# Kernel optimization log

Hardware: AMD Instinct MI355X
Metric: run time of the kernel (lower is better)

Reference implementation:

```python
import jax, jax.numpy as jnp
import numpy as np

HEADS = 4

def _axial_attn(xs, wqkv, wproj, bproj, heads=HEADS):
    # xs: [B', C, L]; wqkv: [3C, C]; wproj: [C, C]; bproj: [C]
    Bp, C, L = xs.shape
    hd = C // heads
    scale = hd ** -0.5
    qkv = jnp.einsum('oc,bcl->bol', wqkv, xs)  # [B', 3C, L]
    q, k, v = jnp.split(qkv, 3, axis=1)
    q = q.reshape(Bp, heads, hd, L)
    k = k.reshape(Bp, heads, hd, L)
    v = v.reshape(Bp, heads, hd, L)
    attn = jax.nn.softmax(jnp.einsum('bhdi,bhdj->bhij', q, k) * scale, axis=-1)
    out = jnp.einsum('bhij,bhdj->bhdi', attn, v).reshape(Bp, C, L)
    return jnp.einsum('oc,bcl->bol', wproj, out) + bproj[None, :, None]

def setup_inputs() -> dict:
    key = jax.random.key(0)
    ks = jax.random.split(key, 7)
    B, C, H, W = 8, 128, 128, 128
    return {
        'x': jax.random.normal(ks[0], (B, C, H, W), dtype=jnp.float32),
        'wqkv_h': jax.random.normal(ks[1], (3 * C, C), dtype=jnp.float32) * 0.05,
        'wproj_h': jax.random.normal(ks[2], (C, C), dtype=jnp.float32) * 0.05,
        'bproj_h': jax.random.normal(ks[3], (C,), dtype=jnp.float32) * 0.05,
        'wqkv_w': jax.random.normal(ks[4], (3 * C, C), dtype=jnp.float32) * 0.05,
        'wproj_w': jax.random.normal(ks[5], (C, C), dtype=jnp.float32) * 0.05,
        'bproj_w': jax.random.normal(ks[6], (C,), dtype=jnp.float32) * 0.05,
    }

def reference(x, wqkv_h, wproj_h, bproj_h, wqkv_w, wproj_w, bproj_w):
    B, C, H, W = x.shape
    # height pass: rows become batch, attend along W
    xh = x.transpose(0, 2, 1, 3).reshape(B * H, C, W)
    xh = _axial_attn(xh, wqkv_h, wproj_h, bproj_h)
    xh = xh.reshape(B, H, C, W).transpose(0, 2, 1, 3)
    # width pass: cols become batch, attend along H
    xw = x.transpose(0, 3, 1, 2).reshape(B * W, C, H)
    xw = _axial_attn(xw, wqkv_w, wproj_w, bproj_w)
    xw = xw.reshape(B, W, C, H).transpose(0, 2, 3, 1)
    return (xh + xw) / 2
```

## Files before the change

kernel.cpp:

```cpp
#include <hip/hip_runtime.h>
#include <hip/hip_bf16.h>
#include <stdint.h>

typedef __attribute__((ext_vector_type(8))) short short8v;
typedef __attribute__((ext_vector_type(4))) float f32x4;
typedef unsigned short u16;
typedef unsigned int u32;

__device__ __align__(16) u16 g_xTw[8u * 128u * 128u * 128u];
__device__ __align__(16) u16 g_W2[8u * 128u * 128u * 128u];
__device__ __align__(16) u16 g_wqkvP[2u * 49152u];
__device__ __align__(16) u16 g_wpP[2u * 16384u];

#define XST_OFF 0
#define QT_OFF  32768
#define KT_OFF  43008
#define VH_OFF  53248
#define OT_OFF  61952
#define SMEM_BYTES 72192

__device__ __forceinline__ u16 f2bf(float f) {
    u32 b = __float_as_uint(f);
    b += 0x7FFFu + ((b >> 16) & 1u);
    return (u16)(b >> 16);
}
__device__ __forceinline__ u32 pk2(float a, float b) {
    __hip_bfloat162 h = __float22bfloat162_rn(make_float2(a, b));
    union { __hip_bfloat162 h; u32 u; } cv; cv.h = h; return cv.u;
}
__device__ __forceinline__ float bf2f(u16 u) {
    return __uint_as_float(((u32)u) << 16);
}

__global__ __launch_bounds__(512)
void prep_weights(const float* __restrict__ wqkv_h, const float* __restrict__ wproj_h,
                  const float* __restrict__ wqkv_w, const float* __restrict__ wproj_w)
{
    const float QSC = 0.17677669529663687f;
    int id = blockIdx.x * 512 + threadIdx.x;
    if (id < 12288) {
        int p = id / 6144, i2 = id % 6144;
        int h = i2 / 1536, i3 = i2 % 1536;
        int t = i3 / 256,  i4 = i3 % 256;
        int kk = i4 / 64,  lane = i4 % 64;
        int cc = lane & 15, qq = lane >> 4;
        int r96 = t * 16 + cc;
        int g = r96 >> 5, rl = r96 & 31;
        const float* src = (p == 0 ? wqkv_h : wqkv_w) + (g * 128 + h * 32 + rl) * 128 + kk * 32 + qq * 8;
        float4 a = *(const float4*)src;
        float4 c = *(const float4*)(src + 4);
        float s = (g == 0) ? QSC : 1.0f;
        *(uint4*)(g_wqkvP + (size_t)id * 8) =
            make_uint4(pk2(a.x * s, a.y * s), pk2(a.z * s, a.w * s),
                       pk2(c.x * s, c.y * s), pk2(c.z * s, c.w * s));
    } else {
        int id2 = id - 12288;
        int p = id2 / 2048, i2 = id2 % 2048;
        int h = i2 / 512,  i3 = i2 % 512;
        int t = i3 / 64,   lane = i3 % 64;
        int cc = lane & 15, qq = lane >> 4;
        int o = t * 16 + cc;
        const float* src = (p == 0 ? wproj_h : wproj_w) + o * 128 + h * 32 + qq * 8;
        float4 a = *(const float4*)src;
        float4 c = *(const float4*)(src + 4);
        *(uint4*)(g_wpP + (size_t)id2 * 8) =
            make_uint4(pk2(a.x, a.y), pk2(a.z, a.w), pk2(c.x, c.y), pk2(c.z, c.w));
    }
}

__global__ __launch_bounds__(256)
void transpose_x(const float* __restrict__ x)
{
    __shared__ char tsm[32768];
    const int b = blockIdx.x >> 6;
    const int hp = blockIdx.x & 63;
    const int tid = threadIdx.x;
    for (int hh = 0; hh < 2; ++hh) {
        const int h = hp * 2 + hh;
        #pragma unroll
        for (int it = 0; it < 16; ++it) {
            int task = it * 256 + tid;
            int w = task & 127, c4 = task >> 7;
            const float* p = x + (size_t)b * 2097152 + (c4 * 4) * 16384 + h * 128 + w;
            u32 u0 = pk2(p[0], p[16384]);
            u32 u1 = pk2(p[2 * 16384], p[3 * 16384]);
            int off = w * 256 + ((((c4 >> 1) << 4) ^ ((w & 7) << 4)) | ((c4 & 1) << 3));
            *(uint2*)(tsm + off) = make_uint2(u0, u1);
        }
        __syncthreads();
        #pragma unroll
        for (int it = 0; it < 8; ++it) {
            int i = it * 256 + tid;
            int w = i >> 4, c8 = i & 15;
            uint4 v = *(const uint4*)(tsm + w * 256 + ((c8 << 4) ^ ((w & 7) << 4)));
            size_t ds = ((size_t)(b * 128 + w) * 128 + h) * 128 + (((c8 << 4) ^ ((h & 7) << 4)) >> 1);
            *(uint4*)(g_xTw + ds) = v;
        }
        __syncthreads();
    }
}

template<int GATHER, int DMODE>
__global__ __launch_bounds__(512, 4)
void attn_kernel(const float* __restrict__ srcx, int pass,
                 const float* __restrict__ bias, float* __restrict__ out)
{
    extern __shared__ char smem[];
    const int t    = threadIdx.x;
    const int lane = t & 63;
    const int wv   = t >> 6;
    const int cc   = lane & 15;
    const int qq   = lane >> 4;
    const int b    = blockIdx.x >> 7;
    const int row  = blockIdx.x & 127;
    const f32x4 zf4 = (f32x4){0.f, 0.f, 0.f, 0.f};

    if constexpr (GATHER) {
        #pragma unroll
        for (int it = 0; it < 4; ++it) {
            int task = t + 512 * it;
            int l = task & 127, c8 = task >> 7;
            const float* p = srcx + (size_t)b * 2097152 + (c8 * 8) * 16384 + row * 128 + l;
            u32 u0 = pk2(p[0], p[16384]);
            u32 u1 = pk2(p[2 * 16384], p[3 * 16384]);
            u32 u2 = pk2(p[4 * 16384], p[5 * 16384]);
            u32 u3 = pk2(p[6 * 16384], p[7 * 16384]);
            *(uint4*)(smem + XST_OFF + l * 256 + ((c8 * 16) ^ ((l & 7) << 4))) = make_uint4(u0, u1, u2, u3);
        }
    } else {
        const u16* slab = g_xTw + (size_t)(b * 128 + row) * 16384;
        #pragma unroll
        for (int it = 0; it < 4; ++it) {
            int idx = t + 512 * it;
            *(uint4*)(smem + XST_OFF + idx * 16) = *(const uint4*)(slab + idx * 8);
        }
    }

    float biasr[4];
    #pragma unroll
    for (int r = 0; r < 4; ++r) biasr[r] = bias[wv * 16 + 4 * qq + r];

    f32x4 yacc[8];
    #pragma unroll
    for (int i = 0; i < 8; ++i) yacc[i] = zf4;

    __syncthreads();

    const int og = wv & 1;
    const int lg = wv >> 1;

    for (int h = 0; h < 4; ++h) {
        const u16* wb  = g_wqkvP + (size_t)(pass * 4 + h) * 12288;
        const u16* wpb = g_wpP   + (size_t)(pass * 4 + h) * 4096 + (wv * 64 + lane) * 8;

        {
            f32x4 acc[3][2];
            #pragma unroll
            for (int ot = 0; ot < 3; ++ot)
                #pragma unroll
                for (int lt = 0; lt < 2; ++lt) acc[ot][lt] = zf4;
            #pragma unroll
            for (int kk = 0; kk < 4; ++kk) {
                short8v A[3], Bf[2];
                #pragma unroll
                for (int ot = 0; ot < 3; ++ot)
                    A[ot] = *(const short8v*)(wb + (((og * 3 + ot) * 4 + kk) * 64 + lane) * 8);
                #pragma unroll
                for (int lt = 0; lt < 2; ++lt) {
                    int l = lg * 32 + lt * 16 + cc;
                    Bf[lt] = *(const short8v*)(smem + XST_OFF + l * 256 + (((kk * 64 + qq * 16)) ^ ((l & 7) << 4)));
                }
                #pragma unroll
                for (int ot = 0; ot < 3; ++ot)
                    #pragma unroll
                    for (int lt = 0; lt < 2; ++lt)
                        acc[ot][lt] = __builtin_amdgcn_mfma_f32_16x16x32_bf16(A[ot], Bf[lt], acc[ot][lt], 0, 0, 0);
            }
            #pragma unroll
            for (int ot = 0; ot < 3; ++ot) {
                int got = og * 3 + ot;
                #pragma unroll
                for (int lt = 0; lt < 2; ++lt) {
                    int l0 = (lg * 2 + lt) * 16 + cc;
                    f32x4 v = acc[ot][lt];
                    if (got < 2) {
                        *(uint2*)(smem + QT_OFF + l0 * 80 + (got * 16 + 4 * qq) * 2) =
                            make_uint2(pk2(v[0], v[1]), pk2(v[2], v[3]));
                    } else if (got < 4) {
                        *(uint2*)(smem + KT_OFF + l0 * 80 + ((got - 2) * 16 + 4 * qq) * 2) =
                            make_uint2(pk2(v[0], v[1]), pk2(v[2], v[3]));
                    } else {
                        int d0 = (got - 4) * 16 + 4 * qq;
                        #pragma unroll
                        for (int r = 0; r < 4; ++r)
                            *(u16*)(smem + VH_OFF + (d0 + r) * 272 + l0 * 2) = f2bf(v[r]);
                    }
                }
            }
        }
        __syncthreads();

        f32x4 sacc[8];
        {
            short8v aq = *(const short8v*)(smem + QT_OFF + (wv * 16 + cc) * 80 + qq * 16);
            #pragma unroll
            for (int jt = 0; jt < 8; ++jt) {
                short8v bk = *(const short8v*)(smem + KT_OFF + (jt * 16 + cc) * 80 + qq * 16);
                sacc[jt] = __builtin_amdgcn_mfma_f32_16x16x32_bf16(bk, aq, zf4, 0, 0, 0);
            }
        }
        float mx = -3.4e38f;
        #pragma unroll
        for (int jt = 0; jt < 8; ++jt)
            #pragma unroll
            for (int r = 0; r < 4; ++r) mx = fmaxf(mx, sacc[jt][r]);
        mx = fmaxf(mx, __shfl_xor(mx, 16));
        mx = fmaxf(mx, __shfl_xor(mx, 32));
        float sm = 0.f;
        #pragma unroll
        for (int jt = 0; jt < 8; ++jt)
            #pragma unroll
            for (int r = 0; r < 4; ++r) {
                float p = exp2f((sacc[jt][r] - mx) * 1.4426950408889634f);
                sacc[jt][r] = p;
                sm += p;
            }
        sm += __shfl_xor(sm, 16);
        sm += __shfl_xor(sm, 32);
        float rden = 1.0f / sm;
        u32 u[8][2];
        #pragma unroll
        for (int jt = 0; jt < 8; ++jt) {
            u[jt][0] = pk2(sacc[jt][0], sacc[jt][1]);
            u[jt][1] = pk2(sacc[jt][2], sacc[jt][3]);
        }

        f32x4 oacc[2] = {zf4, zf4};
        const int base = cc + ((qq & 1) << 5);
        const bool hiT = (qq >> 1) != 0;
        #pragma unroll
        for (int kt = 0; kt < 4; ++kt) {
            int a0 = __shfl((int)u[2 * kt][0], base),      a1 = __shfl((int)u[2 * kt][1], base);
            int a2 = __shfl((int)u[2 * kt][0], base + 16), a3 = __shfl((int)u[2 * kt][1], base + 16);
            int b0 = __shfl((int)u[2 * kt + 1][0], base),      b1 = __shfl((int)u[2 * kt + 1][1], base);
            int b2 = __shfl((int)u[2 * kt + 1][0], base + 16), b3 = __shfl((int)u[2 * kt + 1][1], base + 16);
            union { uint4 u4; short8v s8; } pf;
            pf.u4 = make_uint4((u32)(hiT ? b0 : a0), (u32)(hiT ? b1 : a1),
                               (u32)(hiT ? b2 : a2), (u32)(hiT ? b3 : a3));
            #pragma unroll
            for (int dt = 0; dt < 2; ++dt) {
                short8v vf = *(const short8v*)(smem + VH_OFF + (dt * 16 + cc) * 272 + kt * 64 + qq * 16);
                oacc[dt] = __builtin_amdgcn_mfma_f32_16x16x32_bf16(vf, pf.s8, oacc[dt], 0, 0, 0);
            }
        }
        #pragma unroll
        for (int dt = 0; dt < 2; ++dt) {
            *(uint2*)(smem + OT_OFF + (wv * 16 + cc) * 80 + (dt * 16 + 4 * qq) * 2) =
                make_uint2(pk2(oacc[dt][0] * rden, oacc[dt][1] * rden),
                           pk2(oacc[dt][2] * rden, oacc[dt][3] * rden));
        }
        __syncthreads();

        {
            short8v aw = *(const short8v*)wpb;
            #pragma unroll
            for (int it = 0; it < 8; ++it) {
                short8v of = *(const short8v*)(smem + OT_OFF + (it * 16 + cc) * 80 + qq * 16);
                yacc[it] = __builtin_amdgcn_mfma_f32_16x16x32_bf16(aw, of, yacc[it], 0, 0, 0);
            }
        }
    }

    #pragma unroll
    for (int it = 0; it < 8; ++it) {
        #pragma unroll
        for (int r = 0; r < 4; ++r) {
            float y = (yacc[it][r] + biasr[r]) * 0.5f;
            int o = wv * 16 + 4 * qq + r;
            int l = it * 16 + cc;
            size_t idx = ((size_t)(b * 128 + o) * 128 + row) * 128 + l;
            if constexpr (DMODE == 0) out[idx] = y;
            else                      g_W2[idx] = f2bf(y);
        }
    }
}

__global__ __launch_bounds__(256)
void merge_w(float* __restrict__ out)
{
    __shared__ char msm[128 * 264];
    const int b = blockIdx.x >> 7;
    const int o = blockIdx.x & 127;
    const int tid = threadIdx.x;
    const u16* slab = g_W2 + (size_t)(b * 128 + o) * 16384;
    #pragma unroll
    for (int it = 0; it < 8; ++it) {
        int i = it * 256 + tid;
        int w = i >> 4, h8 = i & 15;
        *(uint4*)(msm + w * 264 + h8 * 16) = *(const uint4*)(slab + w * 128 + h8 * 8);
    }
    __syncthreads();
    float* op = out + (size_t)(b * 128 + o) * 16384;
    #pragma unroll
    for (int it = 0; it < 8; ++it) {
        int i = it * 256 + tid;
        int h = i >> 4, w8 = i & 15;
        float f[8];
        #pragma unroll
        for (int k = 0; k < 8; ++k)
            f[k] = bf2f(*(const u16*)(msm + (w8 * 8 + k) * 264 + h * 2));
        float* dp = op + h * 128 + w8 * 8;
        float4 v0 = *(float4*)dp;
        float4 v1 = *(float4*)(dp + 4);
        v0.x += f[0]; v0.y += f[1]; v0.z += f[2]; v0.w += f[3];
        v1.x += f[4]; v1.y += f[5]; v1.z += f[6]; v1.w += f[7];
        *(float4*)dp = v0;
        *(float4*)(dp + 4) = v1;
    }
}

extern "C" void kernel_launch(void* const* d_in, const int* in_sizes, int n_in,
                              void* d_out, int out_size, void* d_ws, size_t ws_size,
                              hipStream_t stream)
{
    const float* x       = (const float*)d_in[0];
    const float* wqkv_h  = (const float*)d_in[1];
    const float* wproj_h = (const float*)d_in[2];
    const float* bproj_h = (const float*)d_in[3];
    const float* wqkv_w  = (const float*)d_in[4];
    const float* wproj_w = (const float*)d_in[5];
    const float* bproj_w = (const float*)d_in[6];
    float* out = (float*)d_out;

    (void)hipFuncSetAttribute((const void*)attn_kernel<1, 0>,
                              hipFuncAttributeMaxDynamicSharedMemorySize, SMEM_BYTES);
    (void)hipFuncSetAttribute((const void*)attn_kernel<0, 1>,
                              hipFuncAttributeMaxDynamicSharedMemorySize, SMEM_BYTES);

    prep_weights<<<dim3(32), dim3(512), 0, stream>>>(wqkv_h, wproj_h, wqkv_w, wproj_w);
    transpose_x<<<dim3(512), dim3(256), 0, stream>>>(x);
    attn_kernel<1, 0><<<dim3(1024), dim3(512), SMEM_BYTES, stream>>>(x, 0, bproj_h, out);
    attn_kernel<0, 1><<<dim3(1024), dim3(512), SMEM_BYTES, stream>>>(nullptr, 1, bproj_w, out);
    merge_w<<<dim3(1024), dim3(256), 0, stream>>>(out);
}
```

Baseline: 182.2 us.

## Merge both axial passes into one launch and stage bf16 height input

The transpose kernel now also writes a bf16 copy of x laid out per (batch,row) for the height pass. Both attention passes then run in a single 2048-block launch that picks pass, bias and destination from the block index, replacing the strided fp32 gather in pass 0 with a contiguous bf16 load. MFMA sections are wrapped in s_setprio raises so waves doing matrix math get issue priority. The cost is an extra 32 MB bf16 write in the transpose kernel, plus runtime branching where template specialisation used to decide pass behaviour.

```diff
diff --git a/kernel.cpp b/kernel.cpp
--- a/kernel.cpp
+++ b/kernel.cpp
@@ -7,10 +7,11 @@
 typedef unsigned short u16;
 typedef unsigned int u32;
 
+__device__ __align__(16) u16 g_xh [8u * 128u * 128u * 128u];
 __device__ __align__(16) u16 g_xTw[8u * 128u * 128u * 128u];
-__device__ __align__(16) u16 g_W2[8u * 128u * 128u * 128u];
+__device__ __align__(16) u16 g_W2 [8u * 128u * 128u * 128u];
 __device__ __align__(16) u16 g_wqkvP[2u * 49152u];
-__device__ __align__(16) u16 g_wpP[2u * 16384u];
+__device__ __align__(16) u16 g_wpP [2u * 16384u];
 
 #define XST_OFF 0
 #define QT_OFF  32768
@@ -91,6 +92,11 @@
         #pragma unroll
         for (int it = 0; it < 8; ++it) {
             int i = it * 256 + tid;
+            *(uint4*)(g_xh + (size_t)(b * 128 + h) * 16384 + i * 8) = *(const uint4*)(tsm + i * 16);
+        }
+        #pragma unroll
+        for (int it = 0; it < 8; ++it) {
+            int i = it * 256 + tid;
             int w = i >> 4, c8 = i & 15;
             uint4 v = *(const uint4*)(tsm + w * 256 + ((c8 << 4) ^ ((w & 7) << 4)));
             size_t ds = ((size_t)(b * 128 + w) * 128 + h) * 128 + (((c8 << 4) ^ ((h & 7) << 4)) >> 1);
@@ -100,10 +106,9 @@
     }
 }
 
-template<int GATHER, int DMODE>
 __global__ __launch_bounds__(512, 4)
-void attn_kernel(const float* __restrict__ srcx, int pass,
-                 const float* __restrict__ bias, float* __restrict__ out)
+void attn_kernel(const float* __restrict__ bias_h, const float* __restrict__ bias_w,
+                 float* __restrict__ out)
 {
     extern __shared__ char smem[];
     const int t    = threadIdx.x;
@@ -111,24 +116,13 @@
     const int wv   = t >> 6;
     const int cc   = lane & 15;
     const int qq   = lane >> 4;
-    const int b    = blockIdx.x >> 7;
+    const int pass = blockIdx.x >> 10;
+    const int b    = (blockIdx.x >> 7) & 7;
     const int row  = blockIdx.x & 127;
     const f32x4 zf4 = (f32x4){0.f, 0.f, 0.f, 0.f};
 
-    if constexpr (GATHER) {
-        #pragma unroll
-        for (int it = 0; it < 4; ++it) {
-            int task = t + 512 * it;
-            int l = task & 127, c8 = task >> 7;
-            const float* p = srcx + (size_t)b * 2097152 + (c8 * 8) * 16384 + row * 128 + l;
-            u32 u0 = pk2(p[0], p[16384]);
-            u32 u1 = pk2(p[2 * 16384], p[3 * 16384]);
-            u32 u2 = pk2(p[4 * 16384], p[5 * 16384]);
-            u32 u3 = pk2(p[6 * 16384], p[7 * 16384]);
-            *(uint4*)(smem + XST_OFF + l * 256 + ((c8 * 16) ^ ((l & 7) << 4))) = make_uint4(u0, u1, u2, u3);
-        }
-    } else {
-        const u16* slab = g_xTw + (size_t)(b * 128 + row) * 16384;
+    {
+        const u16* slab = (pass ? g_xTw : g_xh) + (size_t)(b * 128 + row) * 16384;
         #pragma unroll
         for (int it = 0; it < 4; ++it) {
             int idx = t + 512 * it;
@@ -136,6 +130,7 @@
         }
     }
 
+    const float* bias = pass ? bias_w : bias_h;
     float biasr[4];
     #pragma unroll
     for (int r = 0; r < 4; ++r) biasr[r] = bias[wv * 16 + 4 * qq + r];
@@ -159,6 +154,7 @@
             for (int ot = 0; ot < 3; ++ot)
                 #pragma unroll
                 for (int lt = 0; lt < 2; ++lt) acc[ot][lt] = zf4;
+            __builtin_amdgcn_s_setprio(1);
             #pragma unroll
             for (int kk = 0; kk < 4; ++kk) {
                 short8v A[3], Bf[2];
@@ -176,6 +172,7 @@
                     for (int lt = 0; lt < 2; ++lt)
                         acc[ot][lt] = __builtin_amdgcn_mfma_f32_16x16x32_bf16(A[ot], Bf[lt], acc[ot][lt], 0, 0, 0);
             }
+            __builtin_amdgcn_s_setprio(0);
             #pragma unroll
             for (int ot = 0; ot < 3; ++ot) {
                 int got = og * 3 + ot;
@@ -203,11 +200,13 @@
         f32x4 sacc[8];
         {
             short8v aq = *(const short8v*)(smem + QT_OFF + (wv * 16 + cc) * 80 + qq * 16);
+            __builtin_amdgcn_s_setprio(1);
             #pragma unroll
             for (int jt = 0; jt < 8; ++jt) {
                 short8v bk = *(const short8v*)(smem + KT_OFF + (jt * 16 + cc) * 80 + qq * 16);
                 sacc[jt] = __builtin_amdgcn_mfma_f32_16x16x32_bf16(bk, aq, zf4, 0, 0, 0);
             }
+            __builtin_amdgcn_s_setprio(0);
         }
         float mx = -3.4e38f;
         #pragma unroll
@@ -238,6 +237,7 @@
         f32x4 oacc[2] = {zf4, zf4};
         const int base = cc + ((qq & 1) << 5);
         const bool hiT = (qq >> 1) != 0;
+        __builtin_amdgcn_s_setprio(1);
         #pragma unroll
         for (int kt = 0; kt < 4; ++kt) {
             int a0 = __shfl((int)u[2 * kt][0], base),      a1 = __shfl((int)u[2 * kt][1], base);
@@ -253,6 +253,7 @@
                 oacc[dt] = __builtin_amdgcn_mfma_f32_16x16x32_bf16(vf, pf.s8, oacc[dt], 0, 0, 0);
             }
         }
+        __builtin_amdgcn_s_setprio(0);
         #pragma unroll
         for (int dt = 0; dt < 2; ++dt) {
             *(uint2*)(smem + OT_OFF + (wv * 16 + cc) * 80 + (dt * 16 + 4 * qq) * 2) =
@@ -263,11 +264,13 @@
 
         {
             short8v aw = *(const short8v*)wpb;
+            __builtin_amdgcn_s_setprio(1);
             #pragma unroll
             for (int it = 0; it < 8; ++it) {
                 short8v of = *(const short8v*)(smem + OT_OFF + (it * 16 + cc) * 80 + qq * 16);
                 yacc[it] = __builtin_amdgcn_mfma_f32_16x16x32_bf16(aw, of, yacc[it], 0, 0, 0);
             }
+            __builtin_amdgcn_s_setprio(0);
         }
     }
 
@@ -279,8 +282,8 @@
             int o = wv * 16 + 4 * qq + r;
             int l = it * 16 + cc;
             size_t idx = ((size_t)(b * 128 + o) * 128 + row) * 128 + l;
-            if constexpr (DMODE == 0) out[idx] = y;
-            else                      g_W2[idx] = f2bf(y);
+            if (pass == 0) out[idx] = y;
+            else           g_W2[idx] = f2bf(y);
         }
     }
 }
@@ -332,14 +335,11 @@
     const float* bproj_w = (const float*)d_in[6];
     float* out = (float*)d_out;
 
-    (void)hipFuncSetAttribute((const void*)attn_kernel<1, 0>,
-                              hipFuncAttributeMaxDynamicSharedMemorySize, SMEM_BYTES);
-    (void)hipFuncSetAttribute((const void*)attn_kernel<0, 1>,
+    (void)hipFuncSetAttribute((const void*)attn_kernel,
                               hipFuncAttributeMaxDynamicSharedMemorySize, SMEM_BYTES);
 
     prep_weights<<<dim3(32), dim3(512), 0, stream>>>(wqkv_h, wproj_h, wqkv_w, wproj_w);
     transpose_x<<<dim3(512), dim3(256), 0, stream>>>(x);
-    attn_kernel<1, 0><<<dim3(1024), dim3(512), SMEM_BYTES, stream>>>(x, 0, bproj_h, out);
-    attn_kernel<0, 1><<<dim3(1024), dim3(512), SMEM_BYTES, stream>>>(nullptr, 1, bproj_w, out);
+    attn_kernel<<<dim3(2048), dim3(512), SMEM_BYTES, stream>>>(bproj_h, bproj_w, out);
     merge_w<<<dim3(1024), dim3(256), 0, stream>>>(out);
 }
```

Result: faster. 170.3 us (-6.5%).
